# Kernel tuning notes

Measured on AMD Instinct MI355X. Metric: run time of the kernel, lower is better.

The kernel has to match this reference:

```python
import jax, jax.numpy as jnp
import numpy as np

N_ENTITIES = 200000
N_USERS = 100000
DIM = 64
N_EDGES = 1000000
N_INTER = 1000000
N_REL = 33
N_INTERACTION_TYPES = 8


def segment_softmax(x, seg, num_segments):
    # two-pass numerically stable segment softmax (torch_scatter.scatter_softmax)
    m = jax.ops.segment_max(x, seg, num_segments=num_segments)
    e = jnp.exp(x - m[seg])
    s = jax.ops.segment_sum(e, seg, num_segments=num_segments)
    return e / s[seg]


def setup_inputs() -> dict:
    key = jax.random.key(0)
    ks = jax.random.split(key, 9)
    return {
        "entity_emb": jax.random.normal(ks[0], (N_ENTITIES, DIM), dtype=jnp.float32),
        "user_emb": jax.random.normal(ks[1], (N_USERS, DIM), dtype=jnp.float32),
        "interaction_emb": jax.random.normal(ks[2], (N_INTERACTION_TYPES, DIM), dtype=jnp.float32),
        "relation_emb": jax.random.normal(ks[3], (N_REL, DIM), dtype=jnp.float32),
        "edge_index": jax.random.randint(ks[4], (2, N_EDGES), 0, N_ENTITIES, dtype=jnp.int32),
        "edge_type": jax.random.randint(ks[5], (N_EDGES,), 1, N_REL, dtype=jnp.int32),
        "user_index": jax.random.randint(ks[6], (N_INTER,), 0, N_USERS, dtype=jnp.int32),
        "item_index": jax.random.randint(ks[7], (N_INTER,), 0, N_ENTITIES, dtype=jnp.int32),
        "interact_type": jax.random.randint(ks[8], (N_INTER,), 0, N_INTERACTION_TYPES, dtype=jnp.int32),
    }


def reference(entity_emb, user_emb, interaction_emb, relation_emb,
              edge_index, edge_type, user_index, item_index, interact_type):
    n_entities = entity_emb.shape[0]
    n_users = user_emb.shape[0]
    head, tail = edge_index[0], edge_index[1]

    # --- entity aggregation over KG edges ---
    neigh = entity_emb[tail]                                      # [E, D]
    w1 = jnp.sum(neigh * relation_emb[edge_type - 1], axis=1) / 8.0   # [E]
    w1 = segment_softmax(w1, head, n_entities)[:, None]           # [E, 1]
    entity_agg = jax.ops.segment_sum(neigh * w1, head, num_segments=n_entities)  # [n_entities, D]

    # --- user aggregation over interactions (agg_method='attention') ---
    interact_entity_emb = entity_emb[item_index]                  # [I, D]
    att = jnp.sum(interaction_emb[interact_type] * user_emb[user_index] * interact_entity_emb, axis=1)  # [I]
    att_w = segment_softmax(att, user_index, n_users)[:, None]    # [I, 1]
    user_agg = jax.ops.segment_sum(att_w * interact_entity_emb, user_index, num_segments=n_users)  # [n_users, D]

    return entity_agg, user_agg, att_w, w1
```

## Files before the change

kernel.cpp:

```cpp
#include <hip/hip_runtime.h>
#include <hip/hip_bf16.h>
#include <hip/hip_fp16.h>

#define DIM 64
#define RELS 32
#define SCAN_B 512
#define TILE_V 64

__device__ __forceinline__ unsigned int pk_h2(float a, float b) {
    __half2 h = __float22half2_rn(make_float2(a, b));
    return *reinterpret_cast<unsigned int*>(&h);
}
__device__ __forceinline__ float4 h4_to_f4(uint2 u) {
    __half2 h0 = *reinterpret_cast<__half2*>(&u.x);
    __half2 h1 = *reinterpret_cast<__half2*>(&u.y);
    float2 f0 = __half22float2(h0);
    float2 f1 = __half22float2(h1);
    return make_float4(f0.x, f0.y, f1.x, f1.y);
}

__global__ __launch_bounds__(256, 4) void buildM_deg(
    const float* __restrict__ ent, const float* __restrict__ rel,
    __hip_bfloat16* __restrict__ M, uint2* __restrict__ entH,
    const int* __restrict__ head, const int* __restrict__ uidx,
    unsigned int* __restrict__ deg,
    unsigned char* __restrict__ rank_e, unsigned char* __restrict__ rank_i,
    int nE, int E, int I, int gM) {
    __shared__ float4 entL[TILE_V * 17];
    __shared__ float relS[4][16][33];
    int tx = threadIdx.x;
    int bid = blockIdx.x;
    int g = bid / 7, slot = bid - g * 7;

    if (slot >= 2) {
        int t = (g * 5 + (slot - 2)) * 256 + tx;
        if (t < E) {
            rank_e[t] = (unsigned char)atomicAdd(&deg[head[t]], 1u);
        } else if (t < E + I) {
            int e = t - E;
            rank_i[e] = (unsigned char)atomicAdd(&deg[nE + uidx[e]], 1u);
        }
        return;
    }

    int mb = g * 2 + slot;
    if (mb >= gM) return;
    int vg = tx >> 4, rg = tx & 15;
    int base = mb * TILE_V;
    const float4* rel4 = (const float4*)rel;
    #pragma unroll
    for (int k = 0; k < 2; k++) {
        int idx = tx + k * 256;
        float4 v = rel4[idx];
        int r = idx >> 4, d4 = idx & 15;
        relS[0][d4][r] = v.x; relS[1][d4][r] = v.y;
        relS[2][d4][r] = v.z; relS[3][d4][r] = v.w;
    }
    const float4* ent4 = (const float4*)ent;
    #pragma unroll
    for (int k = 0; k < 4; k++) {
        int idx = tx + k * 256;
        int row = idx >> 4, col = idx & 15;
        int v = base + row;
        float4 val = make_float4(0.f, 0.f, 0.f, 0.f);
        if (v < nE) {
            val = ent4[(size_t)v * 16 + col];
            entH[(size_t)v * 16 + col] = make_uint2(pk_h2(val.x, val.y), pk_h2(val.z, val.w));
        }
        entL[row * 17 + col] = val;
    }
    __syncthreads();

    float acc[4][2] = {{0.f,0.f},{0.f,0.f},{0.f,0.f},{0.f,0.f}};
    int r0 = rg * 2;
    #pragma unroll 2
    for (int d4 = 0; d4 < 16; d4++) {
        float4 a0 = entL[(vg * 4 + 0) * 17 + d4];
        float4 a1 = entL[(vg * 4 + 1) * 17 + d4];
        float4 a2 = entL[(vg * 4 + 2) * 17 + d4];
        float4 a3 = entL[(vg * 4 + 3) * 17 + d4];
        float bx0 = relS[0][d4][r0],     by0 = relS[1][d4][r0];
        float bz0 = relS[2][d4][r0],     bw0 = relS[3][d4][r0];
        float bx1 = relS[0][d4][r0 + 1], by1 = relS[1][d4][r0 + 1];
        float bz1 = relS[2][d4][r0 + 1], bw1 = relS[3][d4][r0 + 1];
        acc[0][0] = fmaf(a0.x,bx0, fmaf(a0.y,by0, fmaf(a0.z,bz0, fmaf(a0.w,bw0, acc[0][0]))));
        acc[1][0] = fmaf(a1.x,bx0, fmaf(a1.y,by0, fmaf(a1.z,bz0, fmaf(a1.w,bw0, acc[1][0]))));
        acc[2][0] = fmaf(a2.x,bx0, fmaf(a2.y,by0, fmaf(a2.z,bz0, fmaf(a2.w,bw0, acc[2][0]))));
        acc[3][0] = fmaf(a3.x,bx0, fmaf(a3.y,by0, fmaf(a3.z,bz0, fmaf(a3.w,bw0, acc[3][0]))));
        acc[0][1] = fmaf(a0.x,bx1, fmaf(a0.y,by1, fmaf(a0.z,bz1, fmaf(a0.w,bw1, acc[0][1]))));
        acc[1][1] = fmaf(a1.x,bx1, fmaf(a1.y,by1, fmaf(a1.z,bz1, fmaf(a1.w,bw1, acc[1][1]))));
        acc[2][1] = fmaf(a2.x,bx1, fmaf(a2.y,by1, fmaf(a2.z,bz1, fmaf(a2.w,bw1, acc[2][1]))));
        acc[3][1] = fmaf(a3.x,bx1, fmaf(a3.y,by1, fmaf(a3.z,bz1, fmaf(a3.w,bw1, acc[3][1]))));
    }
    __hip_bfloat162* M2 = (__hip_bfloat162*)M;
    #pragma unroll
    for (int i = 0; i < 4; i++) {
        int v = base + vg * 4 + i;
        if (v < nE) {
            __hip_bfloat16 h0 = __float2bfloat16(acc[i][0] * 0.125f);
            __hip_bfloat16 h1 = __float2bfloat16(acc[i][1] * 0.125f);
            M2[(size_t)v * 16 + rg] = __halves2bfloat162(h0, h1);
        }
    }
}

__global__ __launch_bounds__(SCAN_B) void scan_partial(
    const unsigned int* __restrict__ deg, unsigned int* __restrict__ part, int n) {
    __shared__ unsigned int lds[SCAN_B];
    int i = blockIdx.x * SCAN_B + threadIdx.x;
    lds[threadIdx.x] = (i < n) ? deg[i] : 0u;
    __syncthreads();
    for (int off = SCAN_B >> 1; off > 0; off >>= 1) {
        if (threadIdx.x < off) lds[threadIdx.x] += lds[threadIdx.x + off];
        __syncthreads();
    }
    if (threadIdx.x == 0) part[blockIdx.x] = lds[0];
}

__global__ __launch_bounds__(1024) void scan_block(unsigned int* __restrict__ part, int nb) {
    __shared__ unsigned int lds[1024];
    int t = threadIdx.x;
    unsigned int v = (t < nb) ? part[t] : 0u;
    lds[t] = v;
    __syncthreads();
    for (int off = 1; off < 1024; off <<= 1) {
        unsigned int x = (t >= off) ? lds[t - off] : 0u;
        __syncthreads();
        lds[t] += x;
        __syncthreads();
    }
    if (t < nb) part[t] = lds[t] - v;
}

__global__ __launch_bounds__(SCAN_B) void scan_final(
    const unsigned int* __restrict__ deg, const unsigned int* __restrict__ part,
    unsigned int* __restrict__ offs, int n) {
    __shared__ unsigned int lds[SCAN_B];
    int t = threadIdx.x;
    int i = blockIdx.x * SCAN_B + t;
    unsigned int v = (i < n) ? deg[i] : 0u;
    lds[t] = v;
    __syncthreads();
    for (int off = 1; off < SCAN_B; off <<= 1) {
        unsigned int x = (t >= off) ? lds[t - off] : 0u;
        __syncthreads();
        lds[t] += x;
        __syncthreads();
    }
    if (i < n) offs[i] = part[blockIdx.x] + lds[t] - v;
}

__global__ __launch_bounds__(256) void scatter32(
    const __hip_bfloat16* __restrict__ M,
    const int* __restrict__ head, const int* __restrict__ tail, const int* __restrict__ etype,
    const int* __restrict__ uidx, const int* __restrict__ iidx, const int* __restrict__ ttype,
    const unsigned char* __restrict__ rank_e, const unsigned char* __restrict__ rank_i,
    const unsigned int* __restrict__ offs,
    unsigned long long* __restrict__ pay64, unsigned int* __restrict__ payu,
    float* __restrict__ e_sc, int E, int I, int nE) {
    int t = blockIdx.x * blockDim.x + threadIdx.x;
    if (t < E) {
        int tl = tail[t];
        float sc = __bfloat162float(M[(size_t)tl * RELS + (etype[t] - 1)]);
        e_sc[t] = sc;
        unsigned int p = offs[head[t]] + rank_e[t];
        unsigned long long v = ((unsigned long long)__float_as_uint(sc) << 32) | (unsigned int)tl;
        __builtin_nontemporal_store(v, &pay64[p]);
    } else if (t < E + I) {
        int e = t - E;
        unsigned int p = offs[nE + uidx[e]] + rank_i[e] - (unsigned)E;
        unsigned int v = (unsigned int)iidx[e] | ((unsigned int)ttype[e] << 27);
        __builtin_nontemporal_store(v, &payu[p]);
    }
}

__global__ __launch_bounds__(256) void fused_agg(
    const uint2* __restrict__ entH, const float* __restrict__ usr,
    const float* __restrict__ itc,
    const unsigned long long* __restrict__ pay64, const unsigned int* __restrict__ payu,
    const unsigned int* __restrict__ deg, const unsigned int* __restrict__ offs,
    float* __restrict__ patt, float2* __restrict__ msum,
    float* __restrict__ aggE, float* __restrict__ aggU,
    int nE, int nU, int E, int gAE) {
    __shared__ float4 itcL[8][16];
    int tx = threadIdx.x;
    int bid = blockIdx.x;

    if (bid < gAE) {
        int t = bid * 256 + tx;
        int h = t >> 4, l = t & 15;
        if (h >= nE) return;
        unsigned int d = deg[h];
        float m = -3.0e38f, s = 0.f, inv = 0.f;
        float4 acc = make_float4(0.f, 0.f, 0.f, 0.f);
        if (d) {
            unsigned int off = offs[h];
            unsigned long long v0 = pay64[off];
            uint2 b0 = entH[(size_t)(unsigned int)(v0 & 0xffffffffu) * 16 + l];
            for (unsigned int j = 0; j < d; j++) {
                unsigned long long v1 = v0; uint2 b1 = b0;
                if (j + 1 < d) {
                    v1 = pay64[off + j + 1];
                    b1 = entH[(size_t)(unsigned int)(v1 & 0xffffffffu) * 16 + l];
                }
                float sc = __uint_as_float((unsigned int)(v0 >> 32));
                float4 a0 = h4_to_f4(b0);
                float mn = fmaxf(m, sc);
                float scale = __expf(m - mn);
                float w = __expf(sc - mn);
                s = s * scale + w;
                acc.x = acc.x * scale + w * a0.x;
                acc.y = acc.y * scale + w * a0.y;
                acc.z = acc.z * scale + w * a0.z;
                acc.w = acc.w * scale + w * a0.w;
                m = mn; v0 = v1; b0 = b1;
            }
            inv = 1.f / s;
        }
        if (l == 0) msum[h] = make_float2(m, inv);
        acc.x *= inv; acc.y *= inv; acc.z *= inv; acc.w *= inv;
        ((float4*)(aggE + (size_t)h * DIM))[l] = acc;
        return;
    }

    if (tx < 128) itcL[tx >> 4][tx & 15] = ((const float4*)itc)[tx];
    __syncthreads();
    int t = (bid - gAE) * 256 + tx;
    int h = t >> 4, l = t & 15;
    if (h >= nU) return;
    int hs = nE + h;
    unsigned int d = deg[hs];
    float m = -3.0e38f, s = 0.f, inv = 0.f;
    float4 acc = make_float4(0.f, 0.f, 0.f, 0.f);
    float4 ur = ((const float4*)(usr + (size_t)h * DIM))[l];
    if (d) {
        unsigned int off = offs[hs] - (unsigned)E;
        unsigned int v0 = payu[off];
        uint2 b0 = entH[(size_t)(v0 & 0x7ffffffu) * 16 + l];
        for (unsigned int j = 0; j < d; j++) {
            unsigned int v1 = v0; uint2 b1 = b0;
            if (j + 1 < d) {
                v1 = payu[off + j + 1];
                b1 = entH[(size_t)(v1 & 0x7ffffffu) * 16 + l];
            }
            float4 a0 = h4_to_f4(b0);
            float4 c = itcL[v0 >> 27][l];
            float p = a0.x * ur.x * c.x + a0.y * ur.y * c.y
                    + a0.z * ur.z * c.z + a0.w * ur.w * c.w;
            p += __shfl_xor(p, 1);
            p += __shfl_xor(p, 2);
            p += __shfl_xor(p, 4);
            p += __shfl_xor(p, 8);
            if (l == 0) patt[off + j] = p;
            float mn = fmaxf(m, p);
            float scale = __expf(m - mn);
            float w = __expf(p - mn);
            s = s * scale + w;
            acc.x = acc.x * scale + w * a0.x;
            acc.y = acc.y * scale + w * a0.y;
            acc.z = acc.z * scale + w * a0.z;
            acc.w = acc.w * scale + w * a0.w;
            m = mn; v0 = v1; b0 = b1;
        }
        inv = 1.f / s;
    }
    if (l == 0) msum[hs] = make_float2(m, inv);
    acc.x *= inv; acc.y *= inv; acc.z *= inv; acc.w *= inv;
    ((float4*)(aggU + (size_t)h * DIM))[l] = acc;
}

__global__ __launch_bounds__(256) void wout(
    const int* __restrict__ head, const int* __restrict__ uidx,
    const float* __restrict__ e_sc, const float* __restrict__ patt,
    const unsigned char* __restrict__ rank_i,
    const unsigned int* __restrict__ offs, const float2* __restrict__ msum,
    float* __restrict__ w1, float* __restrict__ attw, int E, int I, int nE) {
    int t = blockIdx.x * blockDim.x + threadIdx.x;
    if (t < E) {
        float2 mi = msum[head[t]];
        w1[t] = __expf(e_sc[t] - mi.x) * mi.y;
    } else if (t < E + I) {
        int e = t - E; int u = uidx[e];
        float2 mi = msum[nE + u];
        float sc = patt[offs[nE + u] - (unsigned)E + rank_i[e]];
        attw[e] = __expf(sc - mi.x) * mi.y;
    }
}

extern "C" void kernel_launch(void* const* d_in, const int* in_sizes, int n_in,
                              void* d_out, int out_size, void* d_ws, size_t ws_size,
                              hipStream_t stream) {
    const float* ent  = (const float*)d_in[0];
    const float* usr  = (const float*)d_in[1];
    const float* itc  = (const float*)d_in[2];
    const float* rel  = (const float*)d_in[3];
    const int* eidx   = (const int*)d_in[4];
    const int* etype  = (const int*)d_in[5];
    const int* uidx   = (const int*)d_in[6];
    const int* iidx   = (const int*)d_in[7];
    const int* ttype  = (const int*)d_in[8];

    const int E  = in_sizes[4] / 2;
    const int I  = in_sizes[6];
    const int nE = in_sizes[0] / DIM;
    const int nU = in_sizes[1] / DIM;
    const int* head = eidx;
    const int* tail = eidx + E;
    const int NSEG = nE + nU;
    const int NB = (NSEG + SCAN_B - 1) / SCAN_B;

    float* out_entity = (float*)d_out;
    float* out_user   = out_entity + (size_t)nE * DIM;
    float* out_attw   = out_user + (size_t)nU * DIM;
    float* out_w1     = out_attw + I;

    unsigned int* deg       = (unsigned int*)d_ws;
    unsigned int* offs      = deg + NSEG;
    unsigned int* part      = offs + NSEG;
    unsigned long long* pay64 = (unsigned long long*)(part + 1024);
    unsigned int* payu      = (unsigned int*)(pay64 + E);
    float* e_sc             = (float*)(payu + I);
    __hip_bfloat16* M       = (__hip_bfloat16*)(e_sc + E);
    uint2* entH             = (uint2*)(M + (size_t)nE * RELS);
    float2* msum            = (float2*)(entH + (size_t)nE * 16);
    float* patt             = (float*)(msum + NSEG);
    unsigned char* rank_e   = (unsigned char*)(patt + I);
    unsigned char* rank_i   = rank_e + E;

    hipMemsetAsync(deg, 0, (size_t)NSEG * sizeof(unsigned int), stream);

    const int T = 256;
    const int gM  = (nE + TILE_V - 1) / TILE_V;
    const int gD  = (E + I + T - 1) / T;
    const int NG  = ((gM + 1) / 2 > (gD + 4) / 5) ? (gM + 1) / 2 : (gD + 4) / 5;
    const int gAE = (int)(((size_t)nE * 16 + T - 1) / T);
    const int gAU = (int)(((size_t)nU * 16 + T - 1) / T);

    buildM_deg<<<dim3((unsigned)(NG * 7)), T, 0, stream>>>(
        ent, rel, M, entH, head, uidx, deg, rank_e, rank_i, nE, E, I, gM);

    scan_partial<<<dim3((unsigned)NB), SCAN_B, 0, stream>>>(deg, part, NSEG);
    scan_block<<<dim3(1), 1024, 0, stream>>>(part, NB);
    scan_final<<<dim3((unsigned)NB), SCAN_B, 0, stream>>>(deg, part, offs, NSEG);

    scatter32<<<dim3((unsigned)gD), T, 0, stream>>>(
        M, head, tail, etype, uidx, iidx, ttype, rank_e, rank_i, offs,
        pay64, payu, e_sc, E, I, nE);

    fused_agg<<<dim3((unsigned)(gAE + gAU)), T, 0, stream>>>(
        entH, usr, itc, pay64, payu, deg, offs, patt, msum,
        out_entity, out_user, nE, nU, E, gAE);

    wout<<<dim3((unsigned)gD), T, 0, stream>>>(
        head, uidx, e_sc, patt, rank_i, offs, msum, out_w1, out_attw, E, I, nE);
}
```

Measured before the change: 291.6 us.

## Split degree counters into four copies, dual-chain softmax loop, store interaction slots

Degree atomics now go to four separate counter arrays, one per quarter of the edge and interaction range, to cut contention. The scan combines the four copies and emits a per-copy offset, so scatter finds each slot without touching a shared counter. The aggregation loops now run two independent online-softmax chains with deeper prefetch and merge them at the end, to expose more memory-level parallelism. Interaction slots are saved for the output pass, and workspace buffers are aliased (msum/patt reuse the M region). The costs are larger memset and scan traffic and more registers per thread.

```diff
diff --git a/kernel.cpp b/kernel.cpp
--- a/kernel.cpp
+++ b/kernel.cpp
@@ -23,9 +23,9 @@
     const float* __restrict__ ent, const float* __restrict__ rel,
     __hip_bfloat16* __restrict__ M, uint2* __restrict__ entH,
     const int* __restrict__ head, const int* __restrict__ uidx,
-    unsigned int* __restrict__ deg,
+    unsigned int* __restrict__ degS,
     unsigned char* __restrict__ rank_e, unsigned char* __restrict__ rank_i,
-    int nE, int E, int I, int gM) {
+    int nE, int E, int I, int gM, int Q, int NSEG) {
     __shared__ float4 entL[TILE_V * 17];
     __shared__ float relS[4][16][33];
     int tx = threadIdx.x;
@@ -34,11 +34,15 @@
 
     if (slot >= 2) {
         int t = (g * 5 + (slot - 2)) * 256 + tx;
-        if (t < E) {
-            rank_e[t] = (unsigned char)atomicAdd(&deg[head[t]], 1u);
-        } else if (t < E + I) {
-            int e = t - E;
-            rank_i[e] = (unsigned char)atomicAdd(&deg[nE + uidx[e]], 1u);
+        if (t < E + I) {
+            int k = (t >= Q) + (t >= 2 * Q) + (t >= 3 * Q);
+            unsigned int* dk = degS + (size_t)k * NSEG;
+            if (t < E) {
+                rank_e[t] = (unsigned char)atomicAdd(&dk[head[t]], 1u);
+            } else {
+                int e = t - E;
+                rank_i[e] = (unsigned char)atomicAdd(&dk[nE + uidx[e]], 1u);
+            }
         }
         return;
     }
@@ -105,10 +109,12 @@
 }
 
 __global__ __launch_bounds__(SCAN_B) void scan_partial(
-    const unsigned int* __restrict__ deg, unsigned int* __restrict__ part, int n) {
+    const unsigned int* __restrict__ degS, unsigned int* __restrict__ part, int n) {
     __shared__ unsigned int lds[SCAN_B];
     int i = blockIdx.x * SCAN_B + threadIdx.x;
-    lds[threadIdx.x] = (i < n) ? deg[i] : 0u;
+    unsigned int v = 0;
+    if (i < n) v = degS[i] + degS[n + i] + degS[2 * (size_t)n + i] + degS[3 * (size_t)n + i];
+    lds[threadIdx.x] = v;
     __syncthreads();
     for (int off = SCAN_B >> 1; off > 0; off >>= 1) {
         if (threadIdx.x < off) lds[threadIdx.x] += lds[threadIdx.x + off];
@@ -133,13 +139,19 @@
 }
 
 __global__ __launch_bounds__(SCAN_B) void scan_final(
-    const unsigned int* __restrict__ deg, const unsigned int* __restrict__ part,
-    unsigned int* __restrict__ offs, int n) {
+    const unsigned int* __restrict__ degS, const unsigned int* __restrict__ part,
+    unsigned int* __restrict__ offs0, unsigned int* __restrict__ offs123,
+    int n, unsigned int total) {
     __shared__ unsigned int lds[SCAN_B];
     int t = threadIdx.x;
     int i = blockIdx.x * SCAN_B + t;
-    unsigned int v = (i < n) ? deg[i] : 0u;
-    lds[t] = v;
+    unsigned int a0 = 0, a1 = 0, a2 = 0, a3 = 0, tot = 0;
+    if (i < n) {
+        a0 = degS[i]; a1 = degS[n + i];
+        a2 = degS[2 * (size_t)n + i]; a3 = degS[3 * (size_t)n + i];
+        tot = a0 + a1 + a2 + a3;
+    }
+    lds[t] = tot;
     __syncthreads();
     for (int off = 1; off < SCAN_B; off <<= 1) {
         unsigned int x = (t >= off) ? lds[t - off] : 0u;
@@ -147,7 +159,14 @@
         lds[t] += x;
         __syncthreads();
     }
-    if (i < n) offs[i] = part[blockIdx.x] + lds[t] - v;
+    if (i < n) {
+        unsigned int base = part[blockIdx.x] + lds[t] - tot;
+        offs0[i] = base;
+        offs123[i] = base + a0;
+        offs123[(size_t)n + i] = base + a0 + a1;
+        offs123[2 * (size_t)n + i] = base + a0 + a1 + a2;
+    }
+    if (blockIdx.x == 0 && t == 0) offs0[n] = total;
 }
 
 __global__ __launch_bounds__(256) void scatter32(
@@ -155,22 +174,30 @@
     const int* __restrict__ head, const int* __restrict__ tail, const int* __restrict__ etype,
     const int* __restrict__ uidx, const int* __restrict__ iidx, const int* __restrict__ ttype,
     const unsigned char* __restrict__ rank_e, const unsigned char* __restrict__ rank_i,
-    const unsigned int* __restrict__ offs,
+    const unsigned int* __restrict__ offs0, const unsigned int* __restrict__ offs123,
     unsigned long long* __restrict__ pay64, unsigned int* __restrict__ payu,
-    float* __restrict__ e_sc, int E, int I, int nE) {
+    float* __restrict__ e_sc, unsigned int* __restrict__ slotu,
+    int E, int I, int nE, int Q, int NSEG) {
     int t = blockIdx.x * blockDim.x + threadIdx.x;
+    if (t >= E + I) return;
+    int k = (t >= Q) + (t >= 2 * Q) + (t >= 3 * Q);
     if (t < E) {
+        int s = head[t];
+        unsigned int base = (k == 0) ? offs0[s] : offs123[(size_t)(k - 1) * NSEG + s];
         int tl = tail[t];
         float sc = __bfloat162float(M[(size_t)tl * RELS + (etype[t] - 1)]);
         e_sc[t] = sc;
-        unsigned int p = offs[head[t]] + rank_e[t];
+        unsigned int p = base + rank_e[t];
         unsigned long long v = ((unsigned long long)__float_as_uint(sc) << 32) | (unsigned int)tl;
         __builtin_nontemporal_store(v, &pay64[p]);
-    } else if (t < E + I) {
+    } else {
         int e = t - E;
-        unsigned int p = offs[nE + uidx[e]] + rank_i[e] - (unsigned)E;
+        int s = nE + uidx[e];
+        unsigned int base = (k == 0) ? offs0[s] : offs123[(size_t)(k - 1) * NSEG + s];
+        unsigned int p = base + rank_i[e] - (unsigned)E;
         unsigned int v = (unsigned int)iidx[e] | ((unsigned int)ttype[e] << 27);
         __builtin_nontemporal_store(v, &payu[p]);
+        slotu[e] = p;
     }
 }
 
@@ -178,7 +205,7 @@
     const uint2* __restrict__ entH, const float* __restrict__ usr,
     const float* __restrict__ itc,
     const unsigned long long* __restrict__ pay64, const unsigned int* __restrict__ payu,
-    const unsigned int* __restrict__ deg, const unsigned int* __restrict__ offs,
+    const unsigned int* __restrict__ offs0,
     float* __restrict__ patt, float2* __restrict__ msum,
     float* __restrict__ aggE, float* __restrict__ aggU,
     int nE, int nU, int E, int gAE) {
@@ -190,32 +217,50 @@
         int t = bid * 256 + tx;
         int h = t >> 4, l = t & 15;
         if (h >= nE) return;
-        unsigned int d = deg[h];
-        float m = -3.0e38f, s = 0.f, inv = 0.f;
+        unsigned int off = offs0[h];
+        unsigned int d = offs0[h + 1] - off;
+        float m = -3.0e38f, inv = 0.f;
         float4 acc = make_float4(0.f, 0.f, 0.f, 0.f);
         if (d) {
-            unsigned int off = offs[h];
+            float m0 = -3.0e38f, s0 = 0.f, m1 = -3.0e38f, s1 = 0.f;
+            float4 A0 = make_float4(0.f,0.f,0.f,0.f), A1 = make_float4(0.f,0.f,0.f,0.f);
             unsigned long long v0 = pay64[off];
             uint2 b0 = entH[(size_t)(unsigned int)(v0 & 0xffffffffu) * 16 + l];
-            for (unsigned int j = 0; j < d; j++) {
-                unsigned long long v1 = v0; uint2 b1 = b0;
+            unsigned long long v1 = 0; uint2 b1 = b0;
+            if (d > 1) { v1 = pay64[off + 1]; b1 = entH[(size_t)(unsigned int)(v1 & 0xffffffffu) * 16 + l]; }
+            for (unsigned int j = 0; j < d; j += 2) {
+                unsigned long long nv0 = v0, nv1 = v1; uint2 nb0 = b0, nb1 = b1;
+                if (j + 2 < d) { nv0 = pay64[off + j + 2]; nb0 = entH[(size_t)(unsigned int)(nv0 & 0xffffffffu) * 16 + l]; }
+                if (j + 3 < d) { nv1 = pay64[off + j + 3]; nb1 = entH[(size_t)(unsigned int)(nv1 & 0xffffffffu) * 16 + l]; }
+                {
+                    float sc = __uint_as_float((unsigned int)(v0 >> 32));
+                    float mn = fmaxf(m0, sc);
+                    float sca = __expf(m0 - mn), w = __expf(sc - mn);
+                    float4 a = h4_to_f4(b0);
+                    s0 = s0 * sca + w;
+                    A0.x = A0.x * sca + w * a.x; A0.y = A0.y * sca + w * a.y;
+                    A0.z = A0.z * sca + w * a.z; A0.w = A0.w * sca + w * a.w;
+                    m0 = mn;
+                }
                 if (j + 1 < d) {
-                    v1 = pay64[off + j + 1];
-                    b1 = entH[(size_t)(unsigned int)(v1 & 0xffffffffu) * 16 + l];
+                    float sc = __uint_as_float((unsigned int)(v1 >> 32));
+                    float mn = fmaxf(m1, sc);
+                    float sca = __expf(m1 - mn), w = __expf(sc - mn);
+                    float4 a = h4_to_f4(b1);
+                    s1 = s1 * sca + w;
+                    A1.x = A1.x * sca + w * a.x; A1.y = A1.y * sca + w * a.y;
+                    A1.z = A1.z * sca + w * a.z; A1.w = A1.w * sca + w * a.w;
+                    m1 = mn;
                 }
-                float sc = __uint_as_float((unsigned int)(v0 >> 32));
-                float4 a0 = h4_to_f4(b0);
-                float mn = fmaxf(m, sc);
-                float scale = __expf(m - mn);
-                float w = __expf(sc - mn);
-                s = s * scale + w;
-                acc.x = acc.x * scale + w * a0.x;
-                acc.y = acc.y * scale + w * a0.y;
-                acc.z = acc.z * scale + w * a0.z;
-                acc.w = acc.w * scale + w * a0.w;
-                m = mn; v0 = v1; b0 = b1;
+                v0 = nv0; b0 = nb0; v1 = nv1; b1 = nb1;
             }
+            float mn = fmaxf(m0, m1);
+            float e0 = __expf(m0 - mn), e1 = __expf(m1 - mn);
+            float s = s0 * e0 + s1 * e1;
             inv = 1.f / s;
+            acc.x = A0.x * e0 + A1.x * e1; acc.y = A0.y * e0 + A1.y * e1;
+            acc.z = A0.z * e0 + A1.z * e1; acc.w = A0.w * e0 + A1.w * e1;
+            m = mn;
         }
         if (l == 0) msum[h] = make_float2(m, inv);
         acc.x *= inv; acc.y *= inv; acc.z *= inv; acc.w *= inv;
@@ -229,40 +274,65 @@
     int h = t >> 4, l = t & 15;
     if (h >= nU) return;
     int hs = nE + h;
-    unsigned int d = deg[hs];
-    float m = -3.0e38f, s = 0.f, inv = 0.f;
+    unsigned int off = offs0[hs] - (unsigned)E;
+    unsigned int d = offs0[hs + 1] - offs0[hs];
+    float m = -3.0e38f, inv = 0.f;
     float4 acc = make_float4(0.f, 0.f, 0.f, 0.f);
     float4 ur = ((const float4*)(usr + (size_t)h * DIM))[l];
     if (d) {
-        unsigned int off = offs[hs] - (unsigned)E;
+        float m0 = -3.0e38f, s0 = 0.f, m1 = -3.0e38f, s1 = 0.f;
+        float4 A0 = make_float4(0.f,0.f,0.f,0.f), A1 = make_float4(0.f,0.f,0.f,0.f);
         unsigned int v0 = payu[off];
         uint2 b0 = entH[(size_t)(v0 & 0x7ffffffu) * 16 + l];
-        for (unsigned int j = 0; j < d; j++) {
-            unsigned int v1 = v0; uint2 b1 = b0;
+        unsigned int v1 = 0; uint2 b1 = b0;
+        if (d > 1) { v1 = payu[off + 1]; b1 = entH[(size_t)(v1 & 0x7ffffffu) * 16 + l]; }
+        for (unsigned int j = 0; j < d; j += 2) {
+            unsigned int nv0 = v0, nv1 = v1; uint2 nb0 = b0, nb1 = b1;
+            if (j + 2 < d) { nv0 = payu[off + j + 2]; nb0 = entH[(size_t)(nv0 & 0x7ffffffu) * 16 + l]; }
+            if (j + 3 < d) { nv1 = payu[off + j + 3]; nb1 = entH[(size_t)(nv1 & 0x7ffffffu) * 16 + l]; }
+            {
+                float4 a = h4_to_f4(b0);
+                float4 c = itcL[v0 >> 27][l];
+                float p = a.x * ur.x * c.x + a.y * ur.y * c.y
+                        + a.z * ur.z * c.z + a.w * ur.w * c.w;
+                p += __shfl_xor(p, 1);
+                p += __shfl_xor(p, 2);
+                p += __shfl_xor(p, 4);
+                p += __shfl_xor(p, 8);
+                if (l == 0) patt[off + j] = p;
+                float mn = fmaxf(m0, p);
+                float sca = __expf(m0 - mn), w = __expf(p - mn);
+                s0 = s0 * sca + w;
+                A0.x = A0.x * sca + w * a.x; A0.y = A0.y * sca + w * a.y;
+                A0.z = A0.z * sca + w * a.z; A0.w = A0.w * sca + w * a.w;
+                m0 = mn;
+            }
             if (j + 1 < d) {
-                v1 = payu[off + j + 1];
-                b1 = entH[(size_t)(v1 & 0x7ffffffu) * 16 + l];
+                float4 a = h4_to_f4(b1);
+                float4 c = itcL[v1 >> 27][l];
+                float p = a.x * ur.x * c.x + a.y * ur.y * c.y
+                        + a.z * ur.z * c.z + a.w * ur.w * c.w;
+                p += __shfl_xor(p, 1);
+                p += __shfl_xor(p, 2);
+                p += __shfl_xor(p, 4);
+                p += __shfl_xor(p, 8);
+                if (l == 0) patt[off + j + 1] = p;
+                float mn = fmaxf(m1, p);
+                float sca = __expf(m1 - mn), w = __expf(p - mn);
+                s1 = s1 * sca + w;
+                A1.x = A1.x * sca + w * a.x; A1.y = A1.y * sca + w * a.y;
+                A1.z = A1.z * sca + w * a.z; A1.w = A1.w * sca + w * a.w;
+                m1 = mn;
             }
-            float4 a0 = h4_to_f4(b0);
-            float4 c = itcL[v0 >> 27][l];
-            float p = a0.x * ur.x * c.x + a0.y * ur.y * c.y
-                    + a0.z * ur.z * c.z + a0.w * ur.w * c.w;
-            p += __shfl_xor(p, 1);
-            p += __shfl_xor(p, 2);
-            p += __shfl_xor(p, 4);
-            p += __shfl_xor(p, 8);
-            if (l == 0) patt[off + j] = p;
-            float mn = fmaxf(m, p);
-            float scale = __expf(m - mn);
-            float w = __expf(p - mn);
-            s = s * scale + w;
-            acc.x = acc.x * scale + w * a0.x;
-            acc.y = acc.y * scale + w * a0.y;
-            acc.z = acc.z * scale + w * a0.z;
-            acc.w = acc.w * scale + w * a0.w;
-            m = mn; v0 = v1; b0 = b1;
+            v0 = nv0; b0 = nb0; v1 = nv1; b1 = nb1;
         }
+        float mn = fmaxf(m0, m1);
+        float e0 = __expf(m0 - mn), e1 = __expf(m1 - mn);
+        float s = s0 * e0 + s1 * e1;
         inv = 1.f / s;
+        acc.x = A0.x * e0 + A1.x * e1; acc.y = A0.y * e0 + A1.y * e1;
+        acc.z = A0.z * e0 + A1.z * e1; acc.w = A0.w * e0 + A1.w * e1;
+        m = mn;
     }
     if (l == 0) msum[hs] = make_float2(m, inv);
     acc.x *= inv; acc.y *= inv; acc.z *= inv; acc.w *= inv;
@@ -272,18 +342,16 @@
 __global__ __launch_bounds__(256) void wout(
     const int* __restrict__ head, const int* __restrict__ uidx,
     const float* __restrict__ e_sc, const float* __restrict__ patt,
-    const unsigned char* __restrict__ rank_i,
-    const unsigned int* __restrict__ offs, const float2* __restrict__ msum,
+    const unsigned int* __restrict__ slotu, const float2* __restrict__ msum,
     float* __restrict__ w1, float* __restrict__ attw, int E, int I, int nE) {
     int t = blockIdx.x * blockDim.x + threadIdx.x;
     if (t < E) {
         float2 mi = msum[head[t]];
         w1[t] = __expf(e_sc[t] - mi.x) * mi.y;
     } else if (t < E + I) {
-        int e = t - E; int u = uidx[e];
-        float2 mi = msum[nE + u];
-        float sc = patt[offs[nE + u] - (unsigned)E + rank_i[e]];
-        attw[e] = __expf(sc - mi.x) * mi.y;
+        int e = t - E;
+        float2 mi = msum[nE + uidx[e]];
+        attw[e] = __expf(patt[slotu[e]] - mi.x) * mi.y;
     }
 }
 
@@ -308,26 +376,30 @@
     const int* tail = eidx + E;
     const int NSEG = nE + nU;
     const int NB = (NSEG + SCAN_B - 1) / SCAN_B;
+    const int Q = (E + I + 3) / 4;
 
     float* out_entity = (float*)d_out;
     float* out_user   = out_entity + (size_t)nE * DIM;
     float* out_attw   = out_user + (size_t)nU * DIM;
     float* out_w1     = out_attw + I;
 
-    unsigned int* deg       = (unsigned int*)d_ws;
-    unsigned int* offs      = deg + NSEG;
-    unsigned int* part      = offs + NSEG;
+    unsigned int* degS      = (unsigned int*)d_ws;
+    unsigned int* offs0     = degS + 4 * (size_t)NSEG;
+    unsigned int* offs123   = offs0 + NSEG + 2;
+    unsigned int* part      = offs123 + 3 * (size_t)NSEG;
     unsigned long long* pay64 = (unsigned long long*)(part + 1024);
     unsigned int* payu      = (unsigned int*)(pay64 + E);
     float* e_sc             = (float*)(payu + I);
-    __hip_bfloat16* M       = (__hip_bfloat16*)(e_sc + E);
-    uint2* entH             = (uint2*)(M + (size_t)nE * RELS);
-    float2* msum            = (float2*)(entH + (size_t)nE * 16);
+    unsigned int* slotu     = (unsigned int*)(e_sc + E);
+    unsigned int* Mreg      = slotu + I;
+    __hip_bfloat16* M       = (__hip_bfloat16*)Mreg;
+    float2* msum            = (float2*)Mreg;
     float* patt             = (float*)(msum + NSEG);
-    unsigned char* rank_e   = (unsigned char*)(patt + I);
+    uint2* entH             = (uint2*)(Mreg + (size_t)nE * 16);
+    unsigned char* rank_e   = (unsigned char*)(entH + (size_t)nE * 16);
     unsigned char* rank_i   = rank_e + E;
 
-    hipMemsetAsync(deg, 0, (size_t)NSEG * sizeof(unsigned int), stream);
+    hipMemsetAsync(degS, 0, 4 * (size_t)NSEG * sizeof(unsigned int), stream);
 
     const int T = 256;
     const int gM  = (nE + TILE_V - 1) / TILE_V;
@@ -337,20 +409,21 @@
     const int gAU = (int)(((size_t)nU * 16 + T - 1) / T);
 
     buildM_deg<<<dim3((unsigned)(NG * 7)), T, 0, stream>>>(
-        ent, rel, M, entH, head, uidx, deg, rank_e, rank_i, nE, E, I, gM);
-
-    scan_partial<<<dim3((unsigned)NB), SCAN_B, 0, stream>>>(deg, part, NSEG);
+        ent, rel, M, entH, head, uidx, degS, rank_e, rank_i, nE, E, I, gM, Q, NSEG);
+
+    scan_partial<<<dim3((unsigned)NB), SCAN_B, 0, stream>>>(degS, part, NSEG);
     scan_block<<<dim3(1), 1024, 0, stream>>>(part, NB);
-    scan_final<<<dim3((unsigned)NB), SCAN_B, 0, stream>>>(deg, part, offs, NSEG);
+    scan_final<<<dim3((unsigned)NB), SCAN_B, 0, stream>>>(
+        degS, part, offs0, offs123, NSEG, (unsigned)(E + I));
 
     scatter32<<<dim3((unsigned)gD), T, 0, stream>>>(
-        M, head, tail, etype, uidx, iidx, ttype, rank_e, rank_i, offs,
-        pay64, payu, e_sc, E, I, nE);
+        M, head, tail, etype, uidx, iidx, ttype, rank_e, rank_i, offs0, offs123,
+        pay64, payu, e_sc, slotu, E, I, nE, Q, NSEG);
 
     fused_agg<<<dim3((unsigned)(gAE + gAU)), T, 0, stream>>>(
-        entH, usr, itc, pay64, payu, deg, offs, patt, msum,
+        entH, usr, itc, pay64, payu, offs0, patt, msum,
         out_entity, out_user, nE, nU, E, gAE);
 
     wout<<<dim3((unsigned)gD), T, 0, stream>>>(
-        head, uidx, e_sc, patt, rank_i, offs, msum, out_w1, out_attw, E, I, nE);
-}
+        head, uidx, e_sc, patt, slotu, msum, out_w1, out_attw, E, I, nE);
+}
```

After: 297.9 us. 2.2% more time.
